# Performance work log

Hardware: AMD Instinct MI355X
Metric: run time of the kernel (lower is better)

## Reference

```python
import jax, jax.numpy as jnp
import numpy as np

NUM_HEADS = 12


def setup_inputs() -> dict:
    key = jax.random.key(0)
    ks = jax.random.split(key, 5)
    B, N, C = 4, 2048, 768
    s = 0.02
    return {
        "x": jax.random.normal(ks[0], (B, N, C), jnp.float32),
        "qkv_w": jax.random.normal(ks[1], (3 * C, C), jnp.float32) * s,
        "qkv_b": jax.random.normal(ks[2], (3 * C,), jnp.float32) * s,
        "proj_w": jax.random.normal(ks[3], (C, C), jnp.float32) * s,
        "proj_b": jax.random.normal(ks[4], (C,), jnp.float32) * s,
    }


def reference(x, qkv_w, qkv_b, proj_w, proj_b):
    B, N, C = x.shape
    H = NUM_HEADS
    D = C // H
    scale = D ** -0.5
    # qkv projection: [B,N,3C] -> [3,B,H,N,D]
    qkv = (x @ qkv_w.T + qkv_b).reshape(B, N, 3, H, D).transpose(2, 0, 3, 1, 4)
    q, k, v = qkv[0], qkv[1], qkv[2]
    attn = jnp.einsum("bhnd,bhmd->bhnm", q, k) * scale  # [B,H,N,N]
    attn_probs = jax.nn.softmax(attn, axis=-1)
    # dropout p=0 (eval) -> identity
    out = jnp.einsum("bhnm,bhmd->bhnd", attn_probs, v)  # [B,H,N,D]
    out = out.transpose(0, 2, 1, 3).reshape(B, N, C)
    return out @ proj_w.T + proj_b
```

## Files before the change

kernel.cpp:

```cpp
#include <hip/hip_runtime.h>

typedef __attribute__((ext_vector_type(8))) short bf16x8;
typedef __attribute__((ext_vector_type(4))) float f32x4;
typedef __attribute__((ext_vector_type(4))) unsigned int u32x4;
typedef __attribute__((ext_vector_type(2))) unsigned int u32x2;

#define QSCALE 0.1803368801111243f

__device__ inline unsigned short f2bf(float f) {
  union { float f; unsigned u; } v; v.f = f;
  unsigned r = v.u + 0x7fffu + ((v.u >> 16) & 1u);
  return (unsigned short)(r >> 16);
}

__device__ inline unsigned packbf2(float a, float b) {
  union { float f; unsigned u; } va, vb; va.f = a; vb.f = b;
  unsigned ta = va.u + 0x7fffu + ((va.u >> 16) & 1u);
  unsigned tb = vb.u + 0x7fffu + ((vb.u >> 16) & 1u);
  return __builtin_amdgcn_perm(tb, ta, 0x07060302);
}

__device__ inline unsigned cvtpk_bf16(float a, float b) {
  unsigned r;
  asm("v_cvt_pk_bf16_f32 %0, %1, %2" : "=v"(r) : "v"(a), "v"(b));
  return r;
}

__device__ inline void async16(const void* g, void* l) {
  __builtin_amdgcn_global_load_lds(
      (const __attribute__((address_space(1))) unsigned int*)g,
      (__attribute__((address_space(3))) unsigned int*)l, 16, 0, 0);
}

__device__ inline void cast8(const float* __restrict__ s, unsigned short* __restrict__ d) {
  float4 v0 = *(const float4*)s, v1 = *(const float4*)(s + 4);
  u32x4 o;
  o.x = packbf2(v0.x, v0.y); o.y = packbf2(v0.z, v0.w);
  o.z = packbf2(v1.x, v1.y); o.w = packbf2(v1.z, v1.w);
  *(u32x4*)d = o;
}

__global__ __launch_bounds__(256) void cast_x(const float* __restrict__ x,
                                              unsigned short* __restrict__ xs) {
  size_t idx = (size_t)blockIdx.x * 256 + threadIdx.x;
  cast8(x + idx * 8, xs + idx * 8);
}

__global__ __launch_bounds__(256) void cast_w(const float* __restrict__ wq,
                                              const float* __restrict__ wp,
                                              unsigned short* __restrict__ wqs,
                                              unsigned short* __restrict__ wps) {
  int idx = blockIdx.x * 256 + threadIdx.x;
  if (idx < 221184) cast8(wq + (size_t)idx * 8, wqs + (size_t)idx * 8);
  else {
    size_t j = (size_t)(idx - 221184) * 8;
    cast8(wp + j, wps + j);
  }
}

template<int MODE>
__global__ __launch_bounds__(256, MODE == 0 ? 2 : 3) void gemm_lds(
    const unsigned short* __restrict__ A, const unsigned short* __restrict__ B,
    const float* __restrict__ bias,
    unsigned short* __restrict__ oq, unsigned short* __restrict__ ok,
    unsigned short* __restrict__ ov, float* __restrict__ of)
{
  constexpr int NI = (MODE == 0) ? 4 : 2;
  constexpr int TN = NI * 32;
  constexpr int LSTR = 128 * 64 + TN * 64;
  __shared__ __align__(16) unsigned short lds[2][LSTR];
  unsigned short* As = &lds[0][0];
  unsigned short* Bs = &lds[0][128 * 64];

  const int t = threadIdx.x, w = t >> 6, lane = t & 63;
  const int quad = lane >> 4, l16 = lane & 15;
  const int bm = blockIdx.x, bn = blockIdx.y;
  const int wr = w >> 1, wc = w & 1;

  const int r_off = lane >> 3;
  const int kb_lin = (lane & 7) << 4;

  const unsigned short* Ag = A + (size_t)(bm * 128) * 768;
  const unsigned short* Bg = B + (size_t)(bn * TN) * 768;

  const unsigned short* ApA[4]; unsigned short* LpA[4];
#pragma unroll
  for (int i = 0; i < 4; i++) {
    int r = w * 32 + i * 8 + r_off;
    int ks = (kb_lin ^ ((r & 7) << 4)) >> 1;
    ApA[i] = Ag + (size_t)r * 768 + ks;
    LpA[i] = As + (w * 32 + i * 8) * 64 + lane * 8;
  }
  const unsigned short* ApB[NI]; unsigned short* LpB[NI];
#pragma unroll
  for (int i = 0; i < NI; i++) {
    int r = w * (TN / 4) + i * 8 + r_off;
    int ks = (kb_lin ^ ((r & 7) << 4)) >> 1;
    ApB[i] = Bg + (size_t)r * 768 + ks;
    LpB[i] = Bs + (w * (TN / 4) + i * 8) * 64 + lane * 8;
  }

  f32x4 acc[4][NI] = {};
  const int swz = (l16 & 7) << 3;

#pragma unroll
  for (int i = 0; i < 4; i++)  async16(ApA[i], LpA[i]);
#pragma unroll
  for (int i = 0; i < NI; i++) async16(ApB[i], LpB[i]);
  __syncthreads();

  for (int kt = 0; kt < 12; kt++) {
    const int cur = kt & 1;
    if (kt < 11) {
      const int k1 = (kt + 1) * 64;
      const int nb = (cur ^ 1) * LSTR;
#pragma unroll
      for (int i = 0; i < 4; i++)  async16(ApA[i] + k1, LpA[i] + nb);
#pragma unroll
      for (int i = 0; i < NI; i++) async16(ApB[i] + k1, LpB[i] + nb);
    }
    const unsigned short* Ac = As + cur * LSTR;
    const unsigned short* Bc = Bs + cur * LSTR;
#pragma unroll
    for (int kc = 0; kc < 2; kc++) {
      const int ko = (kc * 32 + quad * 8) ^ swz;
      bf16x8 a[4], b[NI];
#pragma unroll
      for (int mi = 0; mi < 4; mi++)
        a[mi] = *(const bf16x8*)&Ac[(wr * 64 + mi * 16 + l16) * 64 + ko];
#pragma unroll
      for (int ni = 0; ni < NI; ni++)
        b[ni] = *(const bf16x8*)&Bc[(wc * (TN / 2) + ni * 16 + l16) * 64 + ko];
#pragma unroll
      for (int mi = 0; mi < 4; mi++)
#pragma unroll
        for (int ni = 0; ni < NI; ni++)
          acc[mi][ni] = __builtin_amdgcn_mfma_f32_16x16x32_bf16(a[mi], b[ni],
                                                                acc[mi][ni], 0, 0, 0);
    }
    __syncthreads();
  }

  const int m_base = bm * 128 + wr * 64;
  if (MODE == 0) {
    const int three = (bn * 128) / 768;
    int hh[NI], dd[NI]; float bb[NI];
#pragma unroll
    for (int ni = 0; ni < NI; ni++) {
      int n_g = bn * 128 + wc * 64 + ni * 16 + l16;
      bb[ni] = bias[n_g];
      int rem = n_g - three * 768;
      hh[ni] = rem >> 6; dd[ni] = rem & 63;
    }
    if (three == 2) {
#pragma unroll
      for (int ni = 0; ni < NI; ni++)
#pragma unroll
        for (int mi = 0; mi < 4; mi++) {
          int m0 = m_base + mi * 16 + (quad << 2);
          int b_ = m0 >> 11, ntok = m0 & 2047;
          u32x2 pv;
          pv.x = cvtpk_bf16(acc[mi][ni][0] + bb[ni], acc[mi][ni][1] + bb[ni]);
          pv.y = cvtpk_bf16(acc[mi][ni][2] + bb[ni], acc[mi][ni][3] + bb[ni]);
          *(u32x2*)(ov + (((size_t)b_ * 12 + hh[ni]) * 64 + dd[ni]) * 2048 + ntok) = pv;
        }
    } else {
      unsigned short* o = (three == 0) ? oq : ok;
      const float sc = (three == 0) ? QSCALE : 1.f;
#pragma unroll
      for (int mi = 0; mi < 4; mi++)
#pragma unroll
        for (int r = 0; r < 4; r++) {
          int m_g = m_base + mi * 16 + (quad << 2) + r;
          int b_ = m_g >> 11, ntok = m_g & 2047;
          size_t rowb = ((size_t)b_ * 12) * 2048;
#pragma unroll
          for (int ni = 0; ni < NI; ni++) {
            float v = (acc[mi][ni][r] + bb[ni]) * sc;
            o[((rowb + (size_t)hh[ni] * 2048 + ntok) << 6) + dd[ni]] = f2bf(v);
          }
        }
    }
  } else {
#pragma unroll
    for (int ni = 0; ni < NI; ni++) {
      int n_g = bn * TN + wc * (TN / 2) + ni * 16 + l16;
      float bs = bias[n_g];
#pragma unroll
      for (int mi = 0; mi < 4; mi++)
#pragma unroll
        for (int r = 0; r < 4; r++) {
          int m_g = m_base + mi * 16 + (quad << 2) + r;
          of[(size_t)m_g * 768 + n_g] = acc[mi][ni][r] + bs;
        }
    }
  }
}

__global__ __launch_bounds__(256, 3) void flash_attn(
    const unsigned short* __restrict__ Qb, const unsigned short* __restrict__ Kb,
    const unsigned short* __restrict__ Vtb, unsigned short* __restrict__ ao)
{
  __shared__ unsigned short Ks[2][4096];
  __shared__ unsigned short Vs[2][4096];
  const int t = threadIdx.x, w = t >> 6, lane = t & 63;
  const int quad = lane >> 4, l16 = lane & 15;
  const int bh = blockIdx.x, qt = blockIdx.y;
  const unsigned short* Qg = Qb + (size_t)bh * 2048 * 64;
  const unsigned short* Kg = Kb + (size_t)bh * 2048 * 64;
  const unsigned short* Vg = Vtb + (size_t)bh * 2048 * 64;

  bf16x8 bq[2][2];
#pragma unroll
  for (int u = 0; u < 2; u++) {
    int qrow = qt * 128 + w * 32 + u * 16 + l16;
#pragma unroll
    for (int h = 0; h < 2; h++)
      bq[u][h] = *(const bf16x8*)(Qg + (size_t)qrow * 64 + h * 32 + quad * 8);
  }

  const int s0 = t, s1 = 256 + t;
  auto gperm = [](int s) { return (s & 0x23) | ((s & 0x0c) << 1) | ((s & 0x10) >> 2); };
  const size_t koff0 = (size_t)gperm(s0 & 63) * 64 + (s0 >> 6) * 8;
  const size_t koff1 = (size_t)gperm(s1 & 63) * 64 + (s1 >> 6) * 8;
  const size_t voff0 = (size_t)(s0 & 63) * 2048 + (s0 >> 6) * 8;
  const size_t voff1 = (size_t)(s1 & 63) * 2048 + (s1 >> 6) * 8;

  const f32x4 z4 = {0.f, 0.f, 0.f, 0.f};
  f32x4 lacc[2] = {z4, z4};
  f32x4 o_acc[2][4];
#pragma unroll
  for (int u = 0; u < 2; u++)
#pragma unroll
    for (int dt = 0; dt < 4; dt++) o_acc[u][dt] = z4;

  async16(Kg + koff0, &Ks[0][s0 * 8]);
  async16(Kg + koff1, &Ks[0][s1 * 8]);
  async16(Vg + voff0, &Vs[0][s0 * 8]);
  async16(Vg + voff1, &Vs[0][s1 * 8]);

  for (int kt = 0; kt < 32; kt++) {
    const int p = kt & 1;
    __syncthreads();
    if (kt < 31) {
      const unsigned short* Kn = Kg + (size_t)(kt + 1) * 4096;
      const unsigned short* Vn = Vg + (size_t)(kt + 1) * 64;
      async16(Kn + koff0, &Ks[p ^ 1][s0 * 8]);
      async16(Kn + koff1, &Ks[p ^ 1][s1 * 8]);
      async16(Vn + voff0, &Vs[p ^ 1][s0 * 8]);
      async16(Vn + voff1, &Vs[p ^ 1][s1 * 8]);
    }
    const unsigned short* Kp = &Ks[p][0];
    const unsigned short* Vp = &Vs[p][0];

    f32x4 sv[2][4];
    __builtin_amdgcn_s_setprio(1);
#pragma unroll
    for (int nt = 0; nt < 4; nt++) {
      bf16x8 k0 = *(const bf16x8*)&Kp[((quad) * 64 + nt * 16 + l16) * 8];
      bf16x8 k1 = *(const bf16x8*)&Kp[((4 + quad) * 64 + nt * 16 + l16) * 8];
#pragma unroll
      for (int u = 0; u < 2; u++) {
        f32x4 s_ = __builtin_amdgcn_mfma_f32_16x16x32_bf16(k0, bq[u][0], z4, 0, 0, 0);
        s_ = __builtin_amdgcn_mfma_f32_16x16x32_bf16(k1, bq[u][1], s_, 0, 0, 0);
        sv[u][nt] = s_;
      }
    }
    __builtin_amdgcn_s_setprio(0);

    union { unsigned u32[8]; bf16x8 v[2]; } pk[2];
#pragma unroll
    for (int u = 0; u < 2; u++) {
#pragma unroll
      for (int nt = 0; nt < 4; nt++) {
        float p0 = __builtin_amdgcn_exp2f(sv[u][nt][0]);
        float p1 = __builtin_amdgcn_exp2f(sv[u][nt][1]);
        float p2 = __builtin_amdgcn_exp2f(sv[u][nt][2]);
        float p3 = __builtin_amdgcn_exp2f(sv[u][nt][3]);
        lacc[u] += (f32x4){p0, p1, p2, p3};
        pk[u].u32[nt * 2]     = cvtpk_bf16(p0, p1);
        pk[u].u32[nt * 2 + 1] = cvtpk_bf16(p2, p3);
      }
    }

    __builtin_amdgcn_s_setprio(1);
#pragma unroll
    for (int cc = 0; cc < 2; cc++) {
#pragma unroll
      for (int dt = 0; dt < 4; dt++) {
        bf16x8 a = *(const bf16x8*)&Vp[((cc * 4 + quad) * 64 + dt * 16 + l16) * 8];
#pragma unroll
        for (int u = 0; u < 2; u++)
          o_acc[u][dt] = __builtin_amdgcn_mfma_f32_16x16x32_bf16(a, pk[u].v[cc], o_acc[u][dt], 0, 0, 0);
      }
    }
    __builtin_amdgcn_s_setprio(0);
  }

  float linv[2];
#pragma unroll
  for (int u = 0; u < 2; u++) {
    float l = (lacc[u][0] + lacc[u][1]) + (lacc[u][2] + lacc[u][3]);
    l += __shfl_xor(l, 16, 64);
    l += __shfl_xor(l, 32, 64);
    linv[u] = 1.f / l;
  }

  const int b_ = bh / 12, h = bh - b_ * 12;
#pragma unroll
  for (int u = 0; u < 2; u++) {
    int row = b_ * 2048 + qt * 128 + w * 32 + u * 16 + l16;
    unsigned short* base = ao + (size_t)row * 768 + h * 64 + (quad << 2);
#pragma unroll
    for (int dt = 0; dt < 4; dt++) {
      u32x2 pv;
      pv.x = cvtpk_bf16(o_acc[u][dt][0] * linv[u], o_acc[u][dt][1] * linv[u]);
      pv.y = cvtpk_bf16(o_acc[u][dt][2] * linv[u], o_acc[u][dt][3] * linv[u]);
      *(u32x2*)(base + dt * 16) = pv;
    }
  }
}

extern "C" void kernel_launch(void* const* d_in, const int* in_sizes, int n_in,
                              void* d_out, int out_size, void* d_ws, size_t ws_size,
                              hipStream_t stream) {
  const float* x      = (const float*)d_in[0];
  const float* qkv_w  = (const float*)d_in[1];
  const float* qkv_b  = (const float*)d_in[2];
  const float* proj_w = (const float*)d_in[3];
  const float* proj_b = (const float*)d_in[4];
  float* out = (float*)d_out;

  unsigned short* ws  = (unsigned short*)d_ws;
  unsigned short* wqs = ws;
  unsigned short* wps = wqs + 1769472;
  unsigned short* xs  = wps + 589824;
  unsigned short* qb  = xs + 6291456;
  unsigned short* kb  = qb + 6291456;
  unsigned short* vtb = kb + 6291456;
  unsigned short* ao  = vtb + 6291456;

  cast_w<<<1152, 256, 0, stream>>>(qkv_w, proj_w, wqs, wps);
  cast_x<<<3072, 256, 0, stream>>>(x, xs);
  gemm_lds<0><<<dim3(64, 18), 256, 0, stream>>>(xs, wqs, qkv_b, qb, kb, vtb, nullptr);
  flash_attn<<<dim3(48, 16), 256, 0, stream>>>(qb, kb, vtb, ao);
  gemm_lds<1><<<dim3(64, 12), 256, 0, stream>>>(ao, wps, proj_b, nullptr, nullptr, nullptr, out);
}
```

Before: 196.3 us.

## Use 8 waves per attention block with one 16-row Q tile each

The flash attention block grows from 256 to 512 threads, so each wave handles one 16-row query tile instead of two while the block still covers 128 query rows. Each thread now loads one K and one V chunk per tile instead of two. This roughly halves per-wave registers and adds waves for latency hiding. In exchange, every wave rereads the same K/V fragments from LDS for half the MFMA work, doubling LDS read traffic per block, and the barrier now spans more waves.

```diff
diff --git a/kernel.cpp b/kernel.cpp
--- a/kernel.cpp
+++ b/kernel.cpp
@@ -197,7 +197,7 @@
   }
 }
 
-__global__ __launch_bounds__(256, 3) void flash_attn(
+__global__ __launch_bounds__(512, 4) void flash_attn(
     const unsigned short* __restrict__ Qb, const unsigned short* __restrict__ Kb,
     const unsigned short* __restrict__ Vtb, unsigned short* __restrict__ ao)
 {
@@ -210,77 +210,59 @@
   const unsigned short* Kg = Kb + (size_t)bh * 2048 * 64;
   const unsigned short* Vg = Vtb + (size_t)bh * 2048 * 64;
 
-  bf16x8 bq[2][2];
-#pragma unroll
-  for (int u = 0; u < 2; u++) {
-    int qrow = qt * 128 + w * 32 + u * 16 + l16;
+  bf16x8 bq[2];
+  {
+    int qrow = qt * 128 + w * 16 + l16;
 #pragma unroll
     for (int h = 0; h < 2; h++)
-      bq[u][h] = *(const bf16x8*)(Qg + (size_t)qrow * 64 + h * 32 + quad * 8);
-  }
-
-  const int s0 = t, s1 = 256 + t;
+      bq[h] = *(const bf16x8*)(Qg + (size_t)qrow * 64 + h * 32 + quad * 8);
+  }
+
   auto gperm = [](int s) { return (s & 0x23) | ((s & 0x0c) << 1) | ((s & 0x10) >> 2); };
-  const size_t koff0 = (size_t)gperm(s0 & 63) * 64 + (s0 >> 6) * 8;
-  const size_t koff1 = (size_t)gperm(s1 & 63) * 64 + (s1 >> 6) * 8;
-  const size_t voff0 = (size_t)(s0 & 63) * 2048 + (s0 >> 6) * 8;
-  const size_t voff1 = (size_t)(s1 & 63) * 2048 + (s1 >> 6) * 8;
+  const size_t koff = (size_t)gperm(t & 63) * 64 + (t >> 6) * 8;
+  const size_t voff = (size_t)(t & 63) * 2048 + (t >> 6) * 8;
 
   const f32x4 z4 = {0.f, 0.f, 0.f, 0.f};
-  f32x4 lacc[2] = {z4, z4};
-  f32x4 o_acc[2][4];
-#pragma unroll
-  for (int u = 0; u < 2; u++)
-#pragma unroll
-    for (int dt = 0; dt < 4; dt++) o_acc[u][dt] = z4;
-
-  async16(Kg + koff0, &Ks[0][s0 * 8]);
-  async16(Kg + koff1, &Ks[0][s1 * 8]);
-  async16(Vg + voff0, &Vs[0][s0 * 8]);
-  async16(Vg + voff1, &Vs[0][s1 * 8]);
+  f32x4 lacc = z4;
+  f32x4 o_acc[4];
+#pragma unroll
+  for (int dt = 0; dt < 4; dt++) o_acc[dt] = z4;
+
+  async16(Kg + koff, &Ks[0][t * 8]);
+  async16(Vg + voff, &Vs[0][t * 8]);
 
   for (int kt = 0; kt < 32; kt++) {
     const int p = kt & 1;
     __syncthreads();
     if (kt < 31) {
-      const unsigned short* Kn = Kg + (size_t)(kt + 1) * 4096;
-      const unsigned short* Vn = Vg + (size_t)(kt + 1) * 64;
-      async16(Kn + koff0, &Ks[p ^ 1][s0 * 8]);
-      async16(Kn + koff1, &Ks[p ^ 1][s1 * 8]);
-      async16(Vn + voff0, &Vs[p ^ 1][s0 * 8]);
-      async16(Vn + voff1, &Vs[p ^ 1][s1 * 8]);
+      async16(Kg + (size_t)(kt + 1) * 4096 + koff, &Ks[p ^ 1][t * 8]);
+      async16(Vg + (size_t)(kt + 1) * 64 + voff, &Vs[p ^ 1][t * 8]);
     }
     const unsigned short* Kp = &Ks[p][0];
     const unsigned short* Vp = &Vs[p][0];
 
-    f32x4 sv[2][4];
+    f32x4 sv[4];
     __builtin_amdgcn_s_setprio(1);
 #pragma unroll
     for (int nt = 0; nt < 4; nt++) {
       bf16x8 k0 = *(const bf16x8*)&Kp[((quad) * 64 + nt * 16 + l16) * 8];
       bf16x8 k1 = *(const bf16x8*)&Kp[((4 + quad) * 64 + nt * 16 + l16) * 8];
-#pragma unroll
-      for (int u = 0; u < 2; u++) {
-        f32x4 s_ = __builtin_amdgcn_mfma_f32_16x16x32_bf16(k0, bq[u][0], z4, 0, 0, 0);
-        s_ = __builtin_amdgcn_mfma_f32_16x16x32_bf16(k1, bq[u][1], s_, 0, 0, 0);
-        sv[u][nt] = s_;
-      }
+      f32x4 s_ = __builtin_amdgcn_mfma_f32_16x16x32_bf16(k0, bq[0], z4, 0, 0, 0);
+      s_ = __builtin_amdgcn_mfma_f32_16x16x32_bf16(k1, bq[1], s_, 0, 0, 0);
+      sv[nt] = s_;
     }
     __builtin_amdgcn_s_setprio(0);
 
-    union { unsigned u32[8]; bf16x8 v[2]; } pk[2];
-#pragma unroll
-    for (int u = 0; u < 2; u++) {
-#pragma unroll
-      for (int nt = 0; nt < 4; nt++) {
-        float p0 = __builtin_amdgcn_exp2f(sv[u][nt][0]);
-        float p1 = __builtin_amdgcn_exp2f(sv[u][nt][1]);
-        float p2 = __builtin_amdgcn_exp2f(sv[u][nt][2]);
-        float p3 = __builtin_amdgcn_exp2f(sv[u][nt][3]);
-        lacc[u] += (f32x4){p0, p1, p2, p3};
-        pk[u].u32[nt * 2]     = cvtpk_bf16(p0, p1);
-        pk[u].u32[nt * 2 + 1] = cvtpk_bf16(p2, p3);
-      }
+    union { unsigned u32[8]; bf16x8 v[2]; } pk;
+#pragma unroll
+    for (int nt = 0; nt < 4; nt++) {
+      float p0 = __builtin_amdgcn_exp2f(sv[nt][0]);
+      float p1 = __builtin_amdgcn_exp2f(sv[nt][1]);
+      float p2 = __builtin_amdgcn_exp2f(sv[nt][2]);
+      float p3 = __builtin_amdgcn_exp2f(sv[nt][3]);
+      lacc += (f32x4){p0, p1, p2, p3};
+      pk.u32[nt * 2]     = cvtpk_bf16(p0, p1);
+      pk.u32[nt * 2 + 1] = cvtpk_bf16(p2, p3);
     }
 
     __builtin_amdgcn_s_setprio(1);
@@ -289,33 +271,26 @@
 #pragma unroll
       for (int dt = 0; dt < 4; dt++) {
         bf16x8 a = *(const bf16x8*)&Vp[((cc * 4 + quad) * 64 + dt * 16 + l16) * 8];
-#pragma unroll
-        for (int u = 0; u < 2; u++)
-          o_acc[u][dt] = __builtin_amdgcn_mfma_f32_16x16x32_bf16(a, pk[u].v[cc], o_acc[u][dt], 0, 0, 0);
+        o_acc[dt] = __builtin_amdgcn_mfma_f32_16x16x32_bf16(a, pk.v[cc], o_acc[dt], 0, 0, 0);
       }
     }
     __builtin_amdgcn_s_setprio(0);
   }
 
-  float linv[2];
-#pragma unroll
-  for (int u = 0; u < 2; u++) {
-    float l = (lacc[u][0] + lacc[u][1]) + (lacc[u][2] + lacc[u][3]);
-    l += __shfl_xor(l, 16, 64);
-    l += __shfl_xor(l, 32, 64);
-    linv[u] = 1.f / l;
-  }
+  float l = (lacc[0] + lacc[1]) + (lacc[2] + lacc[3]);
+  l += __shfl_xor(l, 16, 64);
+  l += __shfl_xor(l, 32, 64);
+  const float linv = 1.f / l;
 
   const int b_ = bh / 12, h = bh - b_ * 12;
-#pragma unroll
-  for (int u = 0; u < 2; u++) {
-    int row = b_ * 2048 + qt * 128 + w * 32 + u * 16 + l16;
+  {
+    int row = b_ * 2048 + qt * 128 + w * 16 + l16;
     unsigned short* base = ao + (size_t)row * 768 + h * 64 + (quad << 2);
 #pragma unroll
     for (int dt = 0; dt < 4; dt++) {
       u32x2 pv;
-      pv.x = cvtpk_bf16(o_acc[u][dt][0] * linv[u], o_acc[u][dt][1] * linv[u]);
-      pv.y = cvtpk_bf16(o_acc[u][dt][2] * linv[u], o_acc[u][dt][3] * linv[u]);
+      pv.x = cvtpk_bf16(o_acc[dt][0] * linv, o_acc[dt][1] * linv);
+      pv.y = cvtpk_bf16(o_acc[dt][2] * linv, o_acc[dt][3] * linv);
       *(u32x2*)(base + dt * 16) = pv;
     }
   }
@@ -343,6 +318,6 @@
   cast_w<<<1152, 256, 0, stream>>>(qkv_w, proj_w, wqs, wps);
   cast_x<<<3072, 256, 0, stream>>>(x, xs);
   gemm_lds<0><<<dim3(64, 18), 256, 0, stream>>>(xs, wqs, qkv_b, qb, kb, vtb, nullptr);
-  flash_attn<<<dim3(48, 16), 256, 0, stream>>>(qb, kb, vtb, ao);
+  flash_attn<<<dim3(48, 16), 512, 0, stream>>>(qb, kb, vtb, ao);
   gemm_lds<1><<<dim3(64, 12), 256, 0, stream>>>(ao, wps, proj_b, nullptr, nullptr, nullptr, out);
 }
```

New measurement: 200.6 us. +2.2%, slower.
